# Kernel optimization log

Hardware: AMD Instinct MI355X
Metric: run time of the kernel (lower is better)

The kernel has to match this reference:

```python
import jax, jax.numpy as jnp
import numpy as np

ROPE_BASE = 10000.0

def rope_2d(x, h, w):
    # x: (b, h, w, c); 2D RoPE, first half of pair-channels rotated by row angle, second by col angle
    b, _, _, c = x.shape
    k_max = c // 4  # c // (2 * num_spatial_dims)
    theta = 1.0 / (ROPE_BASE ** (jnp.arange(k_max, dtype=jnp.float32) / k_max))  # (k_max,)
    ang_h = jnp.arange(h, dtype=jnp.float32)[:, None] * theta  # (h, k_max)
    ang_w = jnp.arange(w, dtype=jnp.float32)[:, None] * theta  # (w, k_max)
    # angles: (h, w, 2*k_max) = cat([i*theta, j*theta], -1)
    angles = jnp.concatenate([
        jnp.broadcast_to(ang_h[:, None, :], (h, w, k_max)),
        jnp.broadcast_to(ang_w[None, :, :], (h, w, k_max)),
    ], axis=-1)
    cos = jnp.cos(angles)  # (h, w, c//2)
    sin = jnp.sin(angles)
    xr = x[..., 0::2]  # consecutive-pair real parts (b,h,w,c//2)
    xi = x[..., 1::2]
    out_r = xr * cos - xi * sin
    out_i = xr * sin + xi * cos
    return jnp.stack([out_r, out_i], axis=-1).reshape(b, h, w, c)

def linear_attention_fwd(x, h, w, qk_w, qk_b, lepe_w, lepe_b, num_heads=4):
    b, n, c = x.shape
    head_dim = c // num_heads
    qk = x @ qk_w.T + qk_b  # (b, n, 2c)
    q, k = qk[..., :c], qk[..., c:]
    v = x
    q = jax.nn.elu(q) + 1.0
    k = jax.nn.elu(k) + 1.0
    q_rope = rope_2d(q.reshape(b, h, w, c), h, w).reshape(b, n, num_heads, head_dim).transpose(0, 2, 1, 3)
    k_rope = rope_2d(k.reshape(b, h, w, c), h, w).reshape(b, n, num_heads, head_dim).transpose(0, 2, 1, 3)
    qh = q.reshape(b, n, num_heads, head_dim).transpose(0, 2, 1, 3)  # (b,H,n,d)
    kh = k.reshape(b, n, num_heads, head_dim).transpose(0, 2, 1, 3)
    vh = v.reshape(b, n, num_heads, head_dim).transpose(0, 2, 1, 3)
    k_mean = kh.mean(axis=2)  # (b,H,d)
    z = 1.0 / (jnp.einsum('bhnd,bhd->bhn', qh, k_mean) + 1e-6)  # (b,H,n)
    inv_n = 1.0 / n
    kv = jnp.einsum('bhnd,bhne->bhde', k_rope, vh) * inv_n  # (b,H,d,d)
    out = jnp.einsum('bhnd,bhde->bhne', q_rope, kv) * z[..., None]  # (b,H,n,d)
    out = out.transpose(0, 2, 1, 3).reshape(b, n, c)
    # LePE: depthwise 3x3 conv on v in NCHW
    v_img = v.reshape(b, h, w, c).transpose(0, 3, 1, 2)  # (b,c,h,w)
    lepe = jax.lax.conv_general_dilated(
        v_img, lepe_w, window_strides=(1, 1), padding='SAME',
        feature_group_count=c, dimension_numbers=('NCHW', 'OIHW', 'NCHW'))
    lepe = lepe + lepe_b[None, :, None, None]
    out = out + lepe.transpose(0, 2, 3, 1).reshape(b, n, c)
    return out.transpose(0, 2, 1).reshape(b, c, h, w)

def setup_inputs() -> dict:
    key = jax.random.key(0)
    ks = jax.random.split(key, 5)
    b, h, w, c = 16, 128, 128, 64
    n = h * w
    x = jax.random.normal(ks[0], (b, n, c), dtype=jnp.float32)
    qk_w = jax.random.normal(ks[1], (2 * c, c), dtype=jnp.float32) * (1.0 / np.sqrt(c))
    qk_b = jax.random.normal(ks[2], (2 * c,), dtype=jnp.float32) * 0.02
    lepe_w = jax.random.normal(ks[3], (c, 1, 3, 3), dtype=jnp.float32) * (1.0 / 3.0)
    lepe_b = jax.random.normal(ks[4], (c,), dtype=jnp.float32) * 0.02
    return {"x": x, "h": h, "w": w, "qk_w": qk_w, "qk_b": qk_b, "lepe_w": lepe_w, "lepe_b": lepe_b}

def reference(x, h, w, qk_w, qk_b, lepe_w, lepe_b):
    return linear_attention_fwd(x, h, w, qk_w, qk_b, lepe_w, lepe_b, num_heads=4)
```

## Files before the change

### kernel.cpp

```cpp
#include <hip/hip_runtime.h>

#define B_   16
#define C_   64
#define HH   128
#define WW   128
#define NN   (HH*WW)
#define PADB 72
#define PADO 66

typedef short short8 __attribute__((ext_vector_type(8)));
typedef float f32x4  __attribute__((ext_vector_type(4)));

#define NEG_L2_10K_OVER16 (-0.8304820237218406f)
#define INV2PI 0.15915494309189535f

__device__ __forceinline__ float act_elu1(float v) {
    return v > 0.f ? v + 1.f : __expf(v);
}
__device__ __forceinline__ short f2bf(float f) {
    union { float f; unsigned u; } v; v.f = f;
    unsigned r = (v.u + 0x7FFFu + ((v.u >> 16) & 1u)) >> 16;
    return (short)r;
}
__device__ __forceinline__ unsigned cvt2bf(float lo, float hi) {
    unsigned r;
    asm("v_cvt_pk_bf16_f32 %0, %1, %2" : "=v"(r) : "v"(lo), "v"(hi));
    return r;
}
__device__ __forceinline__ void hw_sincos(float rev, float* s, float* c) {
    float f = rev - floorf(rev);
    *s = __builtin_amdgcn_sinf(f);
    *c = __builtin_amdgcn_cosf(f);
}

__global__ __launch_bounds__(256) void la_phase1(
    const float* __restrict__ x, const float* __restrict__ qk_w,
    const float* __restrict__ qk_b, float* __restrict__ g_kv,
    float* __restrict__ g_km)
{
    __shared__ __align__(16) char pool[2*64*PADB*2 + 256*4];
    short* sXT = (short*)pool;
    short* sKT = sXT + 64*PADB;
    float* kmp = (float*)(sKT + 64*PADB);

    const int tid  = threadIdx.x;
    const int w    = tid >> 6;
    const int ln   = tid & 15;
    const int quad = (tid >> 4) & 3;
    const int b    = blockIdx.y;
    const int nblk = blockIdx.x;
    const float* xb = x + (size_t)b * (size_t)(NN * C_);

    short8 bk[2][4];
    #pragma unroll
    for (int ks = 0; ks < 2; ++ks)
        #pragma unroll
        for (int nt = 0; nt < 4; ++nt) {
            const float* wp = qk_w + (64 + 16*nt + ln)*C_ + 32*ks + 8*quad;
            float4 w0 = *(const float4*)wp, w1 = *(const float4*)(wp + 4);
            union { unsigned u[4]; short8 s; } uf;
            uf.u[0] = cvt2bf(w0.x, w0.y); uf.u[1] = cvt2bf(w0.z, w0.w);
            uf.u[2] = cvt2bf(w1.x, w1.y); uf.u[3] = cvt2bf(w1.z, w1.w);
            bk[ks][nt] = uf.s;
        }
    float biasK[4];
    #pragma unroll
    for (int nt = 0; nt < 4; ++nt) biasK[nt] = qk_b[64 + 16*nt + ln];

    float th[2];
    #pragma unroll
    for (int i = 0; i < 2; ++i)
        th[i] = exp2f(NEG_L2_10K_OVER16 * (float)(8*i + (ln >> 1))) * INV2PI;
    float sy[2], cy[2];
    #pragma unroll
    for (int i = 0; i < 2; ++i) hw_sincos((float)nblk * th[i], &sy[i], &cy[i]);

    f32x4 acc2 = {0.f, 0.f, 0.f, 0.f};
    float kmacc[4] = {0.f, 0.f, 0.f, 0.f};
    const int p_base = 16*w + 4*quad;

    for (int ck = 0; ck < 2; ++ck) {
        const int n0 = nblk*128 + ck*64;
        if (ck) __syncthreads();
        #pragma unroll
        for (int it = 0; it < 4; ++it) {
            int idx = tid + 256*it;
            int row = idx & 63, k4 = (idx >> 6) << 2;
            float4 xv = *(const float4*)(xb + (size_t)(n0 + row)*C_ + k4);
            unsigned p01 = cvt2bf(xv.x, xv.y), p23 = cvt2bf(xv.z, xv.w);
            sXT[(k4+0)*PADB + row] = (short)p01;
            sXT[(k4+1)*PADB + row] = (short)(p01 >> 16);
            sXT[(k4+2)*PADB + row] = (short)p23;
            sXT[(k4+3)*PADB + row] = (short)(p23 >> 16);
        }
        short8 aF[2];
        #pragma unroll
        for (int ks = 0; ks < 2; ++ks) {
            const float* ap = xb + (size_t)(n0 + 16*w + ln)*C_ + 32*ks + 8*quad;
            float4 a0 = *(const float4*)ap;
            float4 a1 = *(const float4*)(ap + 4);
            union { unsigned u[4]; short8 s; } af;
            af.u[0] = cvt2bf(a0.x, a0.y);
            af.u[1] = cvt2bf(a0.z, a0.w);
            af.u[2] = cvt2bf(a1.x, a1.y);
            af.u[3] = cvt2bf(a1.z, a1.w);
            aF[ks] = af.s;
        }
        f32x4 ak[4];
        #pragma unroll
        for (int nt = 0; nt < 4; ++nt) ak[nt] = (f32x4){0.f,0.f,0.f,0.f};
        #pragma unroll
        for (int ks = 0; ks < 2; ++ks)
            #pragma unroll
            for (int nt = 0; nt < 4; ++nt)
                ak[nt] = __builtin_amdgcn_mfma_f32_16x16x32_bf16(aF[ks], bk[ks][nt], ak[nt], 0, 0, 0);

        const int x0 = ck*64;
        #pragma unroll
        for (int nt = 0; nt < 4; ++nt) {
            const int j = 16*nt + ln;
            const float sgn = (j & 1) ? 1.f : -1.f;
            #pragma unroll
            for (int r = 0; r < 4; ++r) {
                int p_loc = p_base + r;
                float kval = act_elu1(ak[nt][r] + biasK[nt]);
                kmacc[nt] += kval;
                float P = __shfl_xor(kval, 1);
                float s, c;
                if (nt < 2) { s = sy[nt]; c = cy[nt]; }
                else hw_sincos((float)(x0 + p_loc) * th[nt & 1], &s, &c);
                sKT[j*PADB + p_loc] = f2bf(kval*c + sgn*P*s);
            }
        }
        __syncthreads();
        #pragma unroll
        for (int ks = 0; ks < 2; ++ks) {
            short8 a  = *(const short8*)(sKT + (16*w + ln)*PADB + 32*ks + 8*quad);
            short8 bf = *(const short8*)(sXT + (16*w + ln)*PADB + 32*ks + 8*quad);
            acc2 = __builtin_amdgcn_mfma_f32_16x16x32_bf16(a, bf, acc2, 0, 0, 0);
        }
    }

    float* kvb = g_kv + b*1024;
    #pragma unroll
    for (int r = 0; r < 4; ++r)
        atomicAdd(kvb + w*256 + (4*quad + r)*16 + ln, acc2[r]);

    #pragma unroll
    for (int nt = 0; nt < 4; ++nt) {
        float v = kmacc[nt];
        v += __shfl_xor(v, 16);
        v += __shfl_xor(v, 32);
        if ((tid & 63) < 16) kmp[w*64 + 16*nt + ln] = v;
    }
    __syncthreads();
    if (tid < 64)
        atomicAdd(g_km + b*64 + tid,
                  kmp[tid] + kmp[64 + tid] + kmp[128 + tid] + kmp[192 + tid]);
}

__global__ __launch_bounds__(256) void la_phase2(
    const float* __restrict__ x, const float* __restrict__ qk_w,
    const float* __restrict__ qk_b, const float* __restrict__ lepe_w,
    const float* __restrict__ lepe_b, const float* __restrict__ g_kv,
    const float* __restrict__ g_km, float* __restrict__ out)
{
    __shared__ __align__(16) char pool[5120 + 9216 + 16896 + 2304];
    short* sKVB = (short*)pool;
    short* sQ   = (short*)(pool + 5120);
    float* sOut = (float*)(pool + 5120 + 9216);
    float* sWT  = (float*)(pool + 5120 + 9216 + 16896);

    const int tid  = threadIdx.x;
    const int w    = tid >> 6;
    const int ln   = tid & 15;
    const int quad = (tid >> 4) & 3;
    const int b    = blockIdx.y;
    const int n0   = blockIdx.x * 64;
    const float* xb = x + (size_t)b * (size_t)(NN * C_);
    const float inv_n = 1.f / (float)NN;

    for (int idx = tid; idx < 1024; idx += 256) {
        int h = idx >> 8, d = (idx >> 4) & 15, e = idx & 15;
        float v = g_kv[b*1024 + idx] * inv_n;
        int rowb = h*16 + e;
        int kpos  = (h & 1) ? 16 + d : d;
        int kzero = (h & 1) ? d : 16 + d;
        sKVB[rowb*40 + kpos]  = f2bf(v);
        sKVB[rowb*40 + kzero] = 0;
    }
    if (tid < 144) {
        float4 lw = *(const float4*)(lepe_w + tid*4);
        float lwv[4] = {lw.x, lw.y, lw.z, lw.w};
        #pragma unroll
        for (int i = 0; i < 4; ++i) {
            int e = tid*4 + i, ch = e / 9, tap = e - ch*9;
            sWT[tap*64 + ch] = lwv[i];
        }
    }

    short8 wq[2][4];
    #pragma unroll
    for (int ks = 0; ks < 2; ++ks)
        #pragma unroll
        for (int nt = 0; nt < 4; ++nt) {
            const float* wp = qk_w + (16*nt + ln)*C_ + 32*ks + 8*quad;
            float4 w0 = *(const float4*)wp, w1 = *(const float4*)(wp + 4);
            union { unsigned u[4]; short8 s; } uf;
            uf.u[0] = cvt2bf(w0.x, w0.y); uf.u[1] = cvt2bf(w0.z, w0.w);
            uf.u[2] = cvt2bf(w1.x, w1.y); uf.u[3] = cvt2bf(w1.z, w1.w);
            wq[ks][nt] = uf.s;
        }
    float biasq[4], kmv[4];
    #pragma unroll
    for (int nt = 0; nt < 4; ++nt) {
        biasq[nt] = qk_b[16*nt + ln];
        kmv[nt]   = g_km[b*64 + 16*nt + ln];
    }
    short8 aF[2];
    #pragma unroll
    for (int ks = 0; ks < 2; ++ks) {
        const float* ap = xb + (size_t)(n0 + 16*w + ln)*C_ + 32*ks + 8*quad;
        float4 a0 = *(const float4*)ap;
        float4 a1 = *(const float4*)(ap + 4);
        union { unsigned u[4]; short8 s; } af;
        af.u[0] = cvt2bf(a0.x, a0.y);
        af.u[1] = cvt2bf(a0.z, a0.w);
        af.u[2] = cvt2bf(a1.x, a1.y);
        af.u[3] = cvt2bf(a1.z, a1.w);
        aF[ks] = af.s;
    }
    f32x4 aq[4];
    #pragma unroll
    for (int nt = 0; nt < 4; ++nt) aq[nt] = (f32x4){0.f,0.f,0.f,0.f};
    #pragma unroll
    for (int ks = 0; ks < 2; ++ks)
        #pragma unroll
        for (int nt = 0; nt < 4; ++nt)
            aq[nt] = __builtin_amdgcn_mfma_f32_16x16x32_bf16(aF[ks], wq[ks][nt], aq[nt], 0, 0, 0);

    float qv[4][4], dot[4] = {0.f, 0.f, 0.f, 0.f};
    #pragma unroll
    for (int nt = 0; nt < 4; ++nt)
        #pragma unroll
        for (int r = 0; r < 4; ++r) {
            qv[nt][r] = act_elu1(aq[nt][r] + biasq[nt]);
            dot[r] += qv[nt][r] * kmv[nt];
        }
    float zr[4];
    #pragma unroll
    for (int r = 0; r < 4; ++r) {
        float d = dot[r];
        d += __shfl_xor(d, 1);
        d += __shfl_xor(d, 2);
        d += __shfl_xor(d, 4);
        d += __shfl_xor(d, 8);
        zr[r] = 1.f / (d * inv_n + 1e-6f);
    }

    float th[2];
    #pragma unroll
    for (int i = 0; i < 2; ++i)
        th[i] = exp2f(NEG_L2_10K_OVER16 * (float)(8*i + (ln >> 1))) * INV2PI;
    const int ycoord = n0 >> 7;
    const int x0 = n0 & 127;
    float sy[2], cy[2];
    #pragma unroll
    for (int i = 0; i < 2; ++i) hw_sincos((float)ycoord * th[i], &sy[i], &cy[i]);
    const int p_base = 16*w + 4*quad;
    #pragma unroll
    for (int nt = 0; nt < 4; ++nt) {
        const int j = 16*nt + ln;
        const float sgn = (j & 1) ? 1.f : -1.f;
        #pragma unroll
        for (int r = 0; r < 4; ++r) {
            int p_loc = p_base + r;
            float s, c;
            if (nt < 2) { s = sy[nt]; c = cy[nt]; }
            else hw_sincos((float)(x0 + p_loc) * th[nt & 1], &s, &c);
            float P = __shfl_xor(qv[nt][r], 1);
            float qr = (qv[nt][r]*c + sgn*P*s) * zr[r];
            sQ[p_loc*PADB + j] = f2bf(qr);
        }
    }
    __syncthreads();

    f32x4 accq[4];
    #pragma unroll
    for (int h = 0; h < 4; ++h) accq[h] = (f32x4){0.f,0.f,0.f,0.f};
    #pragma unroll
    for (int P2 = 0; P2 < 2; ++P2) {
        short8 a = *(const short8*)(sQ + (16*w + ln)*PADB + 32*P2 + 8*quad);
        #pragma unroll
        for (int hh = 0; hh < 2; ++hh) {
            int h = 2*P2 + hh;
            short8 bf = *(const short8*)(sKVB + (h*16 + ln)*40 + 8*quad);
            accq[h] = __builtin_amdgcn_mfma_f32_16x16x32_bf16(a, bf, accq[h], 0, 0, 0);
        }
    }
    #pragma unroll
    for (int h = 0; h < 4; ++h)
        #pragma unroll
        for (int r = 0; r < 4; ++r)
            sOut[(16*h + ln)*PADO + 16*w + 4*quad + r] = accq[h][r];

    const int cg = tid & 15;
    const int pg = tid >> 4;
    const int p0 = 4*pg;
    const int yy = n0 >> 7, xbase = n0 & 127, gx0 = xbase + p0;
    f32x4 accl[4];
    #pragma unroll
    for (int j = 0; j < 4; ++j) accl[j] = (f32x4){0.f,0.f,0.f,0.f};
    #pragma unroll
    for (int dy = -1; dy <= 1; ++dy) {
        int y2 = yy + dy;
        if ((unsigned)y2 >= HH) continue;
        f32x4 wt0 = *(const f32x4*)(sWT + ((dy+1)*3 + 0)*C_ + 4*cg);
        f32x4 wt1 = *(const f32x4*)(sWT + ((dy+1)*3 + 1)*C_ + 4*cg);
        f32x4 wt2 = *(const f32x4*)(sWT + ((dy+1)*3 + 2)*C_ + 4*cg);
        const float* rp = xb + (size_t)(y2*WW)*C_ + 4*cg;
        f32x4 cb[6];
        #pragma unroll
        for (int jj = 0; jj < 6; ++jj) {
            int col = gx0 - 1 + jj;
            cb[jj] = ((unsigned)col < WW) ? *(const f32x4*)(rp + (size_t)col*C_)
                                          : (f32x4){0.f,0.f,0.f,0.f};
        }
        #pragma unroll
        for (int j = 0; j < 4; ++j)
            accl[j] += cb[j]*wt0 + cb[j+1]*wt1 + cb[j+2]*wt2;
    }
    __syncthreads();
    #pragma unroll
    for (int j = 0; j < 4; ++j)
        #pragma unroll
        for (int i = 0; i < 4; ++i)
            sOut[(4*cg + i)*PADO + p0 + j] += accl[j][i];
    __syncthreads();

    const int ch = tid >> 2, sub = tid & 3, pp0 = 16*sub;
    const float lb = lepe_b[ch];
    float* outp = out + (size_t)b*(size_t)(C_*NN) + (size_t)ch*NN + n0 + pp0;
    #pragma unroll
    for (int g = 0; g < 4; ++g) {
        float2 a0 = *(const float2*)(sOut + ch*PADO + pp0 + 4*g);
        float2 a1 = *(const float2*)(sOut + ch*PADO + pp0 + 4*g + 2);
        float4 o4 = { a0.x + lb, a0.y + lb, a1.x + lb, a1.y + lb };
        *(float4*)(outp + 4*g) = o4;
    }
}

extern "C" void kernel_launch(void* const* d_in, const int* in_sizes, int n_in,
                              void* d_out, int out_size, void* d_ws, size_t ws_size,
                              hipStream_t stream) {
    const float* x      = (const float*)d_in[0];
    const float* qk_w   = (const float*)d_in[3];
    const float* qk_b   = (const float*)d_in[4];
    const float* lepe_w = (const float*)d_in[5];
    const float* lepe_b = (const float*)d_in[6];
    float* out = (float*)d_out;

    float* g_kv = (float*)d_ws;
    float* g_km = g_kv + 16*1024;
    hipMemsetAsync(d_ws, 0, (size_t)(16*1024 + 16*64) * sizeof(float), stream);

    hipLaunchKernelGGL(la_phase1, dim3(128, B_), dim3(256), 0, stream,
                       x, qk_w, qk_b, g_kv, g_km);
    hipLaunchKernelGGL(la_phase2, dim3(256, B_), dim3(256), 0, stream,
                       x, qk_w, qk_b, lepe_w, lepe_b, g_kv, g_km, out);
}
```

Measured before the change: 210.6 us.

## Double-buffer phase1 chunks, swizzle blocks, alias phase2 LDS, fix per-head normalizer

Phase1 now uses two LDS buffer sets: the second 64-row chunk of x is loaded into registers while the first chunk is computed, which overlaps global loads with the MFMA and RoPE work. Both kernels remap block indices with a swizzle and set launch-bound occupancy hints. Phase2 reuses the sKVB/sQ LDS region for sOut behind an added barrier, shrinking LDS so more blocks fit per CU. The hardware revolution-based sin/cos is replaced by __sincosf. The z normalizer is now reduced per head and applied to q before RoPE, which also changes its numerics to match the reference's per-head denominator.

```diff
diff --git a/kernel.cpp b/kernel.cpp
--- a/kernel.cpp
+++ b/kernel.cpp
@@ -12,7 +12,6 @@
 typedef float f32x4  __attribute__((ext_vector_type(4)));
 
 #define NEG_L2_10K_OVER16 (-0.8304820237218406f)
-#define INV2PI 0.15915494309189535f
 
 __device__ __forceinline__ float act_elu1(float v) {
     return v > 0.f ? v + 1.f : __expf(v);
@@ -27,28 +26,79 @@
     asm("v_cvt_pk_bf16_f32 %0, %1, %2" : "=v"(r) : "v"(lo), "v"(hi));
     return r;
 }
-__device__ __forceinline__ void hw_sincos(float rev, float* s, float* c) {
-    float f = rev - floorf(rev);
-    *s = __builtin_amdgcn_sinf(f);
-    *c = __builtin_amdgcn_cosf(f);
-}
-
-__global__ __launch_bounds__(256) void la_phase1(
+
+__device__ __forceinline__ void p1_chunk(
+    const float* __restrict__ xb, int n0, int xbase, const short8 bk[2][4],
+    const float* biasK, const float* sy, const float* cy, const float* th,
+    int w, int ln, int quad, short* sKTb, float* kmacc)
+{
+    short8 aF[2];
+    #pragma unroll
+    for (int ks = 0; ks < 2; ++ks) {
+        const float* ap = xb + (size_t)(n0 + 16*w + ln)*C_ + 32*ks + 8*quad;
+        float4 a0 = *(const float4*)ap, a1 = *(const float4*)(ap + 4);
+        union { unsigned u[4]; short8 s; } af;
+        af.u[0] = cvt2bf(a0.x, a0.y); af.u[1] = cvt2bf(a0.z, a0.w);
+        af.u[2] = cvt2bf(a1.x, a1.y); af.u[3] = cvt2bf(a1.z, a1.w);
+        aF[ks] = af.s;
+    }
+    f32x4 ak[4];
+    #pragma unroll
+    for (int nt = 0; nt < 4; ++nt) ak[nt] = (f32x4){0.f,0.f,0.f,0.f};
+    #pragma unroll
+    for (int ks = 0; ks < 2; ++ks)
+        #pragma unroll
+        for (int nt = 0; nt < 4; ++nt)
+            ak[nt] = __builtin_amdgcn_mfma_f32_16x16x32_bf16(aF[ks], bk[ks][nt], ak[nt], 0, 0, 0);
+    const int p_base = 16*w + 4*quad;
+    #pragma unroll
+    for (int nt = 0; nt < 4; ++nt) {
+        const int j = 16*nt + ln;
+        const float sgn = (j & 1) ? 1.f : -1.f;
+        #pragma unroll
+        for (int r = 0; r < 4; ++r) {
+            int p_loc = p_base + r;
+            float kval = act_elu1(ak[nt][r] + biasK[nt]);
+            kmacc[nt] += kval;
+            float P = __shfl_xor(kval, 1);
+            float s, c;
+            if (nt < 2) { s = sy[nt]; c = cy[nt]; }
+            else __sincosf((float)(xbase + p_loc) * th[nt & 1], &s, &c);
+            sKTb[j*PADB + p_loc] = f2bf(kval*c + sgn*P*s);
+        }
+    }
+}
+
+__device__ __forceinline__ void p1_kv(
+    const short* sKTb, const short* sXTb, int w, int ln, int quad, f32x4* acc2)
+{
+    #pragma unroll
+    for (int ks = 0; ks < 2; ++ks) {
+        short8 a  = *(const short8*)(sKTb + (16*w + ln)*PADB + 32*ks + 8*quad);
+        short8 bf = *(const short8*)(sXTb + (16*w + ln)*PADB + 32*ks + 8*quad);
+        *acc2 = __builtin_amdgcn_mfma_f32_16x16x32_bf16(a, bf, *acc2, 0, 0, 0);
+    }
+}
+
+__global__ __launch_bounds__(256, 4) void la_phase1(
     const float* __restrict__ x, const float* __restrict__ qk_w,
     const float* __restrict__ qk_b, float* __restrict__ g_kv,
     float* __restrict__ g_km)
 {
-    __shared__ __align__(16) char pool[2*64*PADB*2 + 256*4];
-    short* sXT = (short*)pool;
-    short* sKT = sXT + 64*PADB;
-    float* kmp = (float*)(sKT + 64*PADB);
+    __shared__ __align__(16) char pool[4*64*PADB*2 + 256*4];
+    short* sXT0 = (short*)pool;
+    short* sKT0 = sXT0 + 64*PADB;
+    short* sXT1 = sKT0 + 64*PADB;
+    short* sKT1 = sXT1 + 64*PADB;
+    float* kmp  = (float*)(sKT1 + 64*PADB);
 
     const int tid  = threadIdx.x;
     const int w    = tid >> 6;
     const int ln   = tid & 15;
     const int quad = (tid >> 4) & 3;
     const int b    = blockIdx.y;
-    const int nblk = blockIdx.x;
+    const int bx   = blockIdx.x;
+    const int nblk = ((bx & 7) << 4) | (bx >> 3);
     const float* xb = x + (size_t)b * (size_t)(NN * C_);
 
     short8 bk[2][4];
@@ -70,76 +120,48 @@
     float th[2];
     #pragma unroll
     for (int i = 0; i < 2; ++i)
-        th[i] = exp2f(NEG_L2_10K_OVER16 * (float)(8*i + (ln >> 1))) * INV2PI;
+        th[i] = exp2f(NEG_L2_10K_OVER16 * (float)(8*i + (ln >> 1)));
     float sy[2], cy[2];
     #pragma unroll
-    for (int i = 0; i < 2; ++i) hw_sincos((float)nblk * th[i], &sy[i], &cy[i]);
+    for (int i = 0; i < 2; ++i) __sincosf((float)nblk * th[i], &sy[i], &cy[i]);
+
+    const int srow = tid & 63, scol = (tid >> 6) << 2;
+    float4 xv0[4], xv1[4];
+    #pragma unroll
+    for (int it = 0; it < 4; ++it)
+        xv0[it] = *(const float4*)(xb + (size_t)(nblk*128 + srow)*C_ + scol + 16*it);
+    #pragma unroll
+    for (int it = 0; it < 4; ++it) {
+        int k4 = scol + 16*it;
+        unsigned p01 = cvt2bf(xv0[it].x, xv0[it].y), p23 = cvt2bf(xv0[it].z, xv0[it].w);
+        sXT0[(k4+0)*PADB + srow] = (short)p01;
+        sXT0[(k4+1)*PADB + srow] = (short)(p01 >> 16);
+        sXT0[(k4+2)*PADB + srow] = (short)p23;
+        sXT0[(k4+3)*PADB + srow] = (short)(p23 >> 16);
+    }
+    #pragma unroll
+    for (int it = 0; it < 4; ++it)
+        xv1[it] = *(const float4*)(xb + (size_t)(nblk*128 + 64 + srow)*C_ + scol + 16*it);
+    __syncthreads();
 
     f32x4 acc2 = {0.f, 0.f, 0.f, 0.f};
     float kmacc[4] = {0.f, 0.f, 0.f, 0.f};
-    const int p_base = 16*w + 4*quad;
-
-    for (int ck = 0; ck < 2; ++ck) {
-        const int n0 = nblk*128 + ck*64;
-        if (ck) __syncthreads();
-        #pragma unroll
-        for (int it = 0; it < 4; ++it) {
-            int idx = tid + 256*it;
-            int row = idx & 63, k4 = (idx >> 6) << 2;
-            float4 xv = *(const float4*)(xb + (size_t)(n0 + row)*C_ + k4);
-            unsigned p01 = cvt2bf(xv.x, xv.y), p23 = cvt2bf(xv.z, xv.w);
-            sXT[(k4+0)*PADB + row] = (short)p01;
-            sXT[(k4+1)*PADB + row] = (short)(p01 >> 16);
-            sXT[(k4+2)*PADB + row] = (short)p23;
-            sXT[(k4+3)*PADB + row] = (short)(p23 >> 16);
-        }
-        short8 aF[2];
-        #pragma unroll
-        for (int ks = 0; ks < 2; ++ks) {
-            const float* ap = xb + (size_t)(n0 + 16*w + ln)*C_ + 32*ks + 8*quad;
-            float4 a0 = *(const float4*)ap;
-            float4 a1 = *(const float4*)(ap + 4);
-            union { unsigned u[4]; short8 s; } af;
-            af.u[0] = cvt2bf(a0.x, a0.y);
-            af.u[1] = cvt2bf(a0.z, a0.w);
-            af.u[2] = cvt2bf(a1.x, a1.y);
-            af.u[3] = cvt2bf(a1.z, a1.w);
-            aF[ks] = af.s;
-        }
-        f32x4 ak[4];
-        #pragma unroll
-        for (int nt = 0; nt < 4; ++nt) ak[nt] = (f32x4){0.f,0.f,0.f,0.f};
-        #pragma unroll
-        for (int ks = 0; ks < 2; ++ks)
-            #pragma unroll
-            for (int nt = 0; nt < 4; ++nt)
-                ak[nt] = __builtin_amdgcn_mfma_f32_16x16x32_bf16(aF[ks], bk[ks][nt], ak[nt], 0, 0, 0);
-
-        const int x0 = ck*64;
-        #pragma unroll
-        for (int nt = 0; nt < 4; ++nt) {
-            const int j = 16*nt + ln;
-            const float sgn = (j & 1) ? 1.f : -1.f;
-            #pragma unroll
-            for (int r = 0; r < 4; ++r) {
-                int p_loc = p_base + r;
-                float kval = act_elu1(ak[nt][r] + biasK[nt]);
-                kmacc[nt] += kval;
-                float P = __shfl_xor(kval, 1);
-                float s, c;
-                if (nt < 2) { s = sy[nt]; c = cy[nt]; }
-                else hw_sincos((float)(x0 + p_loc) * th[nt & 1], &s, &c);
-                sKT[j*PADB + p_loc] = f2bf(kval*c + sgn*P*s);
-            }
-        }
-        __syncthreads();
-        #pragma unroll
-        for (int ks = 0; ks < 2; ++ks) {
-            short8 a  = *(const short8*)(sKT + (16*w + ln)*PADB + 32*ks + 8*quad);
-            short8 bf = *(const short8*)(sXT + (16*w + ln)*PADB + 32*ks + 8*quad);
-            acc2 = __builtin_amdgcn_mfma_f32_16x16x32_bf16(a, bf, acc2, 0, 0, 0);
-        }
-    }
+
+    p1_chunk(xb, nblk*128, 0, bk, biasK, sy, cy, th, w, ln, quad, sKT0, kmacc);
+    #pragma unroll
+    for (int it = 0; it < 4; ++it) {
+        int k4 = scol + 16*it;
+        unsigned p01 = cvt2bf(xv1[it].x, xv1[it].y), p23 = cvt2bf(xv1[it].z, xv1[it].w);
+        sXT1[(k4+0)*PADB + srow] = (short)p01;
+        sXT1[(k4+1)*PADB + srow] = (short)(p01 >> 16);
+        sXT1[(k4+2)*PADB + srow] = (short)p23;
+        sXT1[(k4+3)*PADB + srow] = (short)(p23 >> 16);
+    }
+    __syncthreads();
+    p1_kv(sKT0, sXT0, w, ln, quad, &acc2);
+    p1_chunk(xb, nblk*128 + 64, 64, bk, biasK, sy, cy, th, w, ln, quad, sKT1, kmacc);
+    __syncthreads();
+    p1_kv(sKT1, sXT1, w, ln, quad, &acc2);
 
     float* kvb = g_kv + b*1024;
     #pragma unroll
@@ -159,24 +181,25 @@
                   kmp[tid] + kmp[64 + tid] + kmp[128 + tid] + kmp[192 + tid]);
 }
 
-__global__ __launch_bounds__(256) void la_phase2(
+__global__ __launch_bounds__(256, 8) void la_phase2(
     const float* __restrict__ x, const float* __restrict__ qk_w,
     const float* __restrict__ qk_b, const float* __restrict__ lepe_w,
     const float* __restrict__ lepe_b, const float* __restrict__ g_kv,
     const float* __restrict__ g_km, float* __restrict__ out)
 {
-    __shared__ __align__(16) char pool[5120 + 9216 + 16896 + 2304];
+    __shared__ __align__(16) char pool[16896 + 2304];
     short* sKVB = (short*)pool;
     short* sQ   = (short*)(pool + 5120);
-    float* sOut = (float*)(pool + 5120 + 9216);
-    float* sWT  = (float*)(pool + 5120 + 9216 + 16896);
+    float* sOut = (float*)pool;
+    float* sWT  = (float*)(pool + 16896);
 
     const int tid  = threadIdx.x;
     const int w    = tid >> 6;
     const int ln   = tid & 15;
     const int quad = (tid >> 4) & 3;
     const int b    = blockIdx.y;
-    const int n0   = blockIdx.x * 64;
+    const int bx   = blockIdx.x;
+    const int n0   = (((bx & 7) << 5) | (bx >> 3)) * 64;
     const float* xb = x + (size_t)b * (size_t)(NN * C_);
     const float inv_n = 1.f / (float)NN;
 
@@ -221,8 +244,7 @@
     #pragma unroll
     for (int ks = 0; ks < 2; ++ks) {
         const float* ap = xb + (size_t)(n0 + 16*w + ln)*C_ + 32*ks + 8*quad;
-        float4 a0 = *(const float4*)ap;
-        float4 a1 = *(const float4*)(ap + 4);
+        float4 a0 = *(const float4*)ap, a1 = *(const float4*)(ap + 4);
         union { unsigned u[4]; short8 s; } af;
         af.u[0] = cvt2bf(a0.x, a0.y);
         af.u[1] = cvt2bf(a0.z, a0.w);
@@ -239,34 +261,29 @@
         for (int nt = 0; nt < 4; ++nt)
             aq[nt] = __builtin_amdgcn_mfma_f32_16x16x32_bf16(aF[ks], wq[ks][nt], aq[nt], 0, 0, 0);
 
-    float qv[4][4], dot[4] = {0.f, 0.f, 0.f, 0.f};
+    float qv[4][4];
     #pragma unroll
     for (int nt = 0; nt < 4; ++nt)
         #pragma unroll
         for (int r = 0; r < 4; ++r) {
-            qv[nt][r] = act_elu1(aq[nt][r] + biasq[nt]);
-            dot[r] += qv[nt][r] * kmv[nt];
-        }
-    float zr[4];
-    #pragma unroll
-    for (int r = 0; r < 4; ++r) {
-        float d = dot[r];
-        d += __shfl_xor(d, 1);
-        d += __shfl_xor(d, 2);
-        d += __shfl_xor(d, 4);
-        d += __shfl_xor(d, 8);
-        zr[r] = 1.f / (d * inv_n + 1e-6f);
-    }
+            float q0 = act_elu1(aq[nt][r] + biasq[nt]);
+            float dp = q0 * kmv[nt];
+            dp += __shfl_xor(dp, 1);
+            dp += __shfl_xor(dp, 2);
+            dp += __shfl_xor(dp, 4);
+            dp += __shfl_xor(dp, 8);
+            qv[nt][r] = q0 / (dp * inv_n + 1e-6f);
+        }
 
     float th[2];
     #pragma unroll
     for (int i = 0; i < 2; ++i)
-        th[i] = exp2f(NEG_L2_10K_OVER16 * (float)(8*i + (ln >> 1))) * INV2PI;
+        th[i] = exp2f(NEG_L2_10K_OVER16 * (float)(8*i + (ln >> 1)));
     const int ycoord = n0 >> 7;
     const int x0 = n0 & 127;
     float sy[2], cy[2];
     #pragma unroll
-    for (int i = 0; i < 2; ++i) hw_sincos((float)ycoord * th[i], &sy[i], &cy[i]);
+    for (int i = 0; i < 2; ++i) __sincosf((float)ycoord * th[i], &sy[i], &cy[i]);
     const int p_base = 16*w + 4*quad;
     #pragma unroll
     for (int nt = 0; nt < 4; ++nt) {
@@ -277,10 +294,9 @@
             int p_loc = p_base + r;
             float s, c;
             if (nt < 2) { s = sy[nt]; c = cy[nt]; }
-            else hw_sincos((float)(x0 + p_loc) * th[nt & 1], &s, &c);
+            else __sincosf((float)(x0 + p_loc) * th[nt & 1], &s, &c);
             float P = __shfl_xor(qv[nt][r], 1);
-            float qr = (qv[nt][r]*c + sgn*P*s) * zr[r];
-            sQ[p_loc*PADB + j] = f2bf(qr);
+            sQ[p_loc*PADB + j] = f2bf(qv[nt][r]*c + sgn*P*s);
         }
     }
     __syncthreads();
@@ -298,6 +314,8 @@
             accq[h] = __builtin_amdgcn_mfma_f32_16x16x32_bf16(a, bf, accq[h], 0, 0, 0);
         }
     }
+    __syncthreads();
+
     #pragma unroll
     for (int h = 0; h < 4; ++h)
         #pragma unroll
```

After: 202.5 us. 1.04x faster.
